# Kernel optimization log

Hardware: AMD Instinct MI355X
Metric: run time of the kernel (lower is better)

The kernel has to match this reference:

```python
import jax, jax.numpy as jnp
import numpy as np

B = 4          # batch (number of point clouds)
NPER = 50000   # voxels per cloud
G = 96         # voxel grid extent per axis
C = 128        # in_channels
R = 2          # reduction_ratio
K = 27         # 3^3 kernel offsets
BN_EPS = 1e-5


def _build_sparse_geometry(seed=0):
    """Unique voxel coords per sample + 27-neighbor kernel map (Minkowski-style)."""
    rng = np.random.default_rng(seed)
    keys_list = []
    for b in range(B):
        loc = rng.choice(G ** 3, NPER, replace=False)
        loc.sort()
        keys_list.append(b * (G ** 3) + loc)
    keys = np.concatenate(keys_list)  # globally sorted (batch-major)
    N = keys.shape[0]
    loc = keys % (G ** 3)
    xs, ys, zs = loc // (G * G), (loc // G) % G, loc % G
    offsets = [(dx, dy, dz) for dx in (-1, 0, 1) for dy in (-1, 0, 1) for dz in (-1, 0, 1)]
    nbr_idx = np.zeros((N, K), np.int32)
    nbr_mask = np.zeros((N, K), bool)
    for k, (dx, dy, dz) in enumerate(offsets):
        inb = ((xs + dx >= 0) & (xs + dx < G) & (ys + dy >= 0) & (ys + dy < G)
               & (zs + dz >= 0) & (zs + dz < G))
        nkey = keys + dx * G * G + dy * G + dz
        pos = np.searchsorted(keys, nkey)
        pos_c = np.clip(pos, 0, N - 1)
        found = inb & (keys[pos_c] == nkey)
        nbr_idx[:, k] = np.where(found, pos_c, 0)
        nbr_mask[:, k] = found
    batch_idx = np.repeat(np.arange(B), NPER).astype(np.int32)
    return nbr_idx, nbr_mask, batch_idx


def setup_inputs() -> dict:
    nbr_idx, nbr_mask, batch_idx = _build_sparse_geometry(0)
    N = B * NPER
    key = jax.random.key(0)
    ks = jax.random.split(key, 8)
    feats = jax.random.normal(ks[0], (N, C), jnp.float32)
    # channel-attention MLP (MinkowskiLinear has bias=True)
    w1 = jax.random.normal(ks[1], (C, C // R), jnp.float32) * (1.0 / np.sqrt(C))
    b1 = jnp.zeros((C // R,), jnp.float32)
    w2 = jax.random.normal(ks[2], (C // R, C), jnp.float32) * (1.0 / np.sqrt(C // R))
    b2 = jnp.zeros((C,), jnp.float32)
    # spatial attention: 3x3x3 sparse conv C->4 (bias=False), BN(4), 1x1x1 conv 4->4
    conv1_w = jax.random.normal(ks[3], (K, C, 4), jnp.float32) * (1.0 / np.sqrt(K * C))
    bn_gamma = jnp.ones((4,), jnp.float32)
    bn_beta = jnp.zeros((4,), jnp.float32)
    conv2_w = jax.random.normal(ks[4], (4, 4), jnp.float32) * 0.5
    return dict(feats=feats, w1=w1, b1=b1, w2=w2, b2=b2, conv1_w=conv1_w,
                bn_gamma=bn_gamma, bn_beta=bn_beta, conv2_w=conv2_w,
                nbr_idx=jnp.asarray(nbr_idx), nbr_mask=jnp.asarray(nbr_mask),
                batch_idx=jnp.asarray(batch_idx), num_batches=B)


def reference(feats, w1, b1, w2, b2, conv1_w, bn_gamma, bn_beta, conv2_w,
              nbr_idx, nbr_mask, batch_idx, num_batches):
    N = feats.shape[0]
    ones = jnp.ones((N,), feats.dtype)
    counts = jax.ops.segment_sum(ones, batch_idx, num_segments=num_batches,
                                 indices_are_sorted=True)  # [B]
    avg_x = jax.ops.segment_sum(feats, batch_idx, num_segments=num_batches,
                                indices_are_sorted=True) / counts[:, None]  # [B,C]
    max_x = jax.ops.segment_max(feats, batch_idx, num_segments=num_batches,
                                indices_are_sorted=True)  # [B,C]
    mlp = lambda z: jax.nn.relu(z @ w1 + b1) @ w2 + b2
    weights = jax.nn.sigmoid(mlp(avg_x) + mlp(max_x))  # [B,C] channel attention
    # sam_mid: per-sample broadcast multiply
    mid = feats * weights[batch_idx]  # [N,C]
    # sparse 3x3x3 conv C->4 via kernel map (gather + thin matmul per offset)
    mask_f = nbr_mask.astype(feats.dtype)
    y = jnp.zeros((N, 4), feats.dtype)
    for k in range(K):
        y = y + (mid[nbr_idx[:, k]] * mask_f[:, k:k + 1]) @ conv1_w[k]
    # BatchNorm (training-mode batch stats, biased var) + ReLU
    mu = jnp.mean(y, axis=0)
    var = jnp.var(y, axis=0)
    y = (y - mu) * jax.lax.rsqrt(var + BN_EPS) * bn_gamma + bn_beta
    y = jax.nn.relu(y)
    # 1x1x1 conv == linear (bias=False), then sigmoid
    final = jax.nn.sigmoid(y @ conv2_w)  # [N,4]
    # sam_output: max over channels -> scalar spatial gate per point
    gate = jnp.max(final, axis=1, keepdims=True)  # [N,1]
    out = mid * gate + mid + feats
    return out
```

## Files before the change

kernel.cpp:

```cpp
#include <hip/hip_runtime.h>

#define C 128
#define K 27
#define BATCHES 4
#define RA_BPB 512
#define CONV_BLOCKS 512
#define CONV_BPB (CONV_BLOCKS / BATCHES)
#define CONV_TPB 1024
#define NWAVES_CONV (CONV_BLOCKS * (CONV_TPB / 64))
#define BN_EPS 1e-5f

typedef __attribute__((ext_vector_type(2))) __fp16 h2;
typedef __attribute__((ext_vector_type(8))) __fp16 h8;

__global__ __launch_bounds__(256) void reduceA_kernel(
    const float* __restrict__ feats, float* __restrict__ psum,
    float* __restrict__ pmax, const unsigned int* __restrict__ mwords,
    int* __restrict__ flag, int NPER) {
  int base = blockIdx.x * 512;
  bool bad = false;
  bad |= (mwords[base + threadIdx.x] > 1u);
  bad |= (mwords[base + 256 + threadIdx.x] > 1u);
  if (__any(bad) && (threadIdx.x & 63) == 0) atomicOr(flag, 1);

  int b = blockIdx.x / RA_BPB, chunk = blockIdx.x % RA_BPB;
  int CH = (NPER + RA_BPB - 1) / RA_BPB;
  int r0 = b * NPER + chunk * CH;
  int r1 = min(b * NPER + NPER, r0 + CH);
  int g = threadIdx.x >> 5;
  int l = threadIdx.x & 31;
  float4 s = make_float4(0.f, 0.f, 0.f, 0.f);
  float4 m = make_float4(-INFINITY, -INFINITY, -INFINITY, -INFINITY);
  int i = r0 + g;
  for (; i + 8 < r1; i += 16) {
    float4 v1 = *(const float4*)(feats + (size_t)i * C + l * 4);
    float4 v2 = *(const float4*)(feats + (size_t)(i + 8) * C + l * 4);
    s.x += v1.x + v2.x; s.y += v1.y + v2.y;
    s.z += v1.z + v2.z; s.w += v1.w + v2.w;
    m.x = fmaxf(m.x, fmaxf(v1.x, v2.x)); m.y = fmaxf(m.y, fmaxf(v1.y, v2.y));
    m.z = fmaxf(m.z, fmaxf(v1.z, v2.z)); m.w = fmaxf(m.w, fmaxf(v1.w, v2.w));
  }
  if (i < r1) {
    float4 v = *(const float4*)(feats + (size_t)i * C + l * 4);
    s.x += v.x; s.y += v.y; s.z += v.z; s.w += v.w;
    m.x = fmaxf(m.x, v.x); m.y = fmaxf(m.y, v.y);
    m.z = fmaxf(m.z, v.z); m.w = fmaxf(m.w, v.w);
  }
  __shared__ float ssum[8][C], smax[8][C];
  *(float4*)&ssum[g][l * 4] = s;
  *(float4*)&smax[g][l * 4] = m;
  __syncthreads();
  if (threadIdx.x < C) {
    int c = threadIdx.x;
    float S = 0.f, M = -INFINITY;
#pragma unroll
    for (int gg = 0; gg < 8; ++gg) {
      S += ssum[gg][c];
      M = fmaxf(M, smax[gg][c]);
    }
    psum[(size_t)blockIdx.x * C + c] = S;
    pmax[(size_t)blockIdx.x * C + c] = M;
  }
}

__global__ __launch_bounds__(256) void reduceB_mlp_kernel(
    const float* __restrict__ psum, const float* __restrict__ pmax,
    const float* __restrict__ w1, const float* __restrict__ b1,
    const float* __restrict__ w2, const float* __restrict__ b2,
    float* __restrict__ wgt, int NPER) {
  int b = blockIdx.x;
  int g = threadIdx.x >> 5, l = threadIdx.x & 31;
  float4 s = make_float4(0.f, 0.f, 0.f, 0.f);
  float4 m = make_float4(-INFINITY, -INFINITY, -INFINITY, -INFINITY);
  for (int j = g; j < RA_BPB; j += 8) {
    size_t base = (size_t)(b * RA_BPB + j) * C + l * 4;
    float4 vs = *(const float4*)(psum + base);
    float4 vm = *(const float4*)(pmax + base);
    s.x += vs.x; s.y += vs.y; s.z += vs.z; s.w += vs.w;
    m.x = fmaxf(m.x, vm.x); m.y = fmaxf(m.y, vm.y);
    m.z = fmaxf(m.z, vm.z); m.w = fmaxf(m.w, vm.w);
  }
  __shared__ float ssum[8][C], smax[8][C];
  *(float4*)&ssum[g][l * 4] = s;
  *(float4*)&smax[g][l * 4] = m;
  __syncthreads();
  __shared__ float avgs[C], mxs[C];
  if (threadIdx.x < C) {
    int c = threadIdx.x;
    float S = 0.f, M = -INFINITY;
#pragma unroll
    for (int gg = 0; gg < 8; ++gg) {
      S += ssum[gg][c];
      M = fmaxf(M, smax[gg][c]);
    }
    avgs[c] = S / (float)NPER;
    mxs[c] = M;
  }
  __syncthreads();
  __shared__ float h1a[64], h1m[64];
  int t = threadIdx.x;
  if (t < 64) {
    float sa = b1[t], sm = b1[t];
    for (int c = 0; c < C; ++c) {
      float wv = w1[c * 64 + t];
      sa += avgs[c] * wv;
      sm += mxs[c] * wv;
    }
    h1a[t] = fmaxf(sa, 0.f);
    h1m[t] = fmaxf(sm, 0.f);
  }
  __syncthreads();
  if (t < C) {
    float za = b2[t], zm = b2[t];
    for (int h = 0; h < 64; ++h) {
      float wv = w2[h * C + t];
      za += h1a[h] * wv;
      zm += h1m[h] * wv;
    }
    float z = za + zm;
    wgt[b * C + t] = 1.f / (1.f + expf(-z));
  }
}

__global__ __launch_bounds__(CONV_TPB, 8) void conv_kernel(
    const float* __restrict__ feats, const float* __restrict__ wgt,
    const float* __restrict__ conv1_w, const int* __restrict__ nbr_idx,
    const void* __restrict__ nbr_mask, const int* __restrict__ flagp,
    float* __restrict__ y, float* __restrict__ bnpart, int N, int NPER) {
  int bat = blockIdx.x / CONV_BPB;
  const float* wgtRow = wgt + bat * C;
  __shared__ __align__(16) h8 wlds[K * 64];
  int tid = threadIdx.x;
  for (int e = tid; e < K * 64; e += CONV_TPB) {
    int l = e & 63;
    float wa = wgtRow[2 * l], wb = wgtRow[2 * l + 1];
    float4 A = ((const float4*)conv1_w)[e * 2];
    float4 B = ((const float4*)conv1_w)[e * 2 + 1];
    h8 w;
    h2 p;
    p = __builtin_amdgcn_cvt_pkrtz(A.x * wa, B.x * wb); w[0] = p[0]; w[1] = p[1];
    p = __builtin_amdgcn_cvt_pkrtz(A.y * wa, B.y * wb); w[2] = p[0]; w[3] = p[1];
    p = __builtin_amdgcn_cvt_pkrtz(A.z * wa, B.z * wb); w[4] = p[0]; w[5] = p[1];
    p = __builtin_amdgcn_cvt_pkrtz(A.w * wa, B.w * wb); w[6] = p[0]; w[7] = p[1];
    wlds[e] = w;
  }
  __syncthreads();

  int lane = tid & 63;
  int g = lane >> 4, cl = lane & 15;
  int gwave = blockIdx.x * (CONV_TPB / 64) + (tid >> 6);
  int wb = (blockIdx.x % CONV_BPB) * (CONV_TPB / 64) + (tid >> 6);
  int wavesPerBatch = CONV_BPB * (CONV_TPB / 64);
  int rpw = (NPER + wavesPerBatch - 1) / wavesPerBatch;
  int rbeg = bat * NPER + wb * rpw;
  int rend = min(bat * NPER + NPER, rbeg + rpw);
  bool byteMode = (*flagp != 0);
  const unsigned char* mb = (const unsigned char*)nbr_mask;
  const int* mi = (const int*)nbr_mask;

  bool mk = false;
  int jl = 0;
  if (rbeg < rend && lane < K) {
    size_t e = (size_t)rbeg * K + lane;
    mk = byteMode ? (mb[e] != 0) : (mi[e] != 0);
    jl = nbr_idx[e];
  }

  float sAcc = 0.f, qAcc = 0.f;

  unsigned balTailN = 0, balTailP = 0;
  int jN = 0, jP = 0, cntN = 0, cntP = 0;
  int k0N = 0, k1N = 0, k2N = 0, k3N = 0, k0P = 0, k1P = 0, k2P = 0, k3P = 0;
  float2 g0N = make_float2(0, 0), g1N = g0N, g2N = g0N, g3N = g0N;
  float2 g0P = g0N, g1P = g0N, g2P = g0N, g3P = g0N;

#define FRONT(iF)                                                           \
  do {                                                                      \
    unsigned bb = (unsigned)__ballot(mk);                                   \
    jN = jl;                                                                \
    mk = false;                                                             \
    if ((iF) + 1 < rend && lane < K) {                                      \
      size_t e = (size_t)((iF) + 1) * K + lane;                             \
      mk = byteMode ? (mb[e] != 0) : (mi[e] != 0);                          \
      jl = nbr_idx[e];                                                      \
    }                                                                       \
    cntN = __popc(bb);                                                      \
    k0N = __ffs(bb) - 1; bb &= bb - 1;                                      \
    k1N = __ffs(bb) - 1; bb &= bb - 1;                                      \
    k2N = __ffs(bb) - 1; bb &= bb - 1;                                      \
    k3N = __ffs(bb) - 1; bb &= bb - 1;                                      \
    balTailN = bb;                                                          \
    int j0 = __shfl(jN, k0N & 63);                                          \
    int j1 = __shfl(jN, k1N & 63);                                          \
    int j2 = __shfl(jN, k2N & 63);                                          \
    int j3 = __shfl(jN, k3N & 63);                                          \
    if (cntN > 0) g0N = *(const float2*)(feats + (size_t)j0 * C + 2 * lane);\
    if (cntN > 1) g1N = *(const float2*)(feats + (size_t)j1 * C + 2 * lane);\
    if (cntN > 2) g2N = *(const float2*)(feats + (size_t)j2 * C + 2 * lane);\
    if (cntN > 3) g3N = *(const float2*)(feats + (size_t)j3 * C + 2 * lane);\
  } while (0)

#define ACCD(ff, kk)                                                        \
  {                                                                         \
    h2 fp = __builtin_amdgcn_cvt_pkrtz(ff.x, ff.y);                         \
    h8 w = wlds[(kk)*64 + lane];                                            \
    h2 w0 = __builtin_shufflevector(w, w, 0, 1);                            \
    h2 w1 = __builtin_shufflevector(w, w, 2, 3);                            \
    h2 w2 = __builtin_shufflevector(w, w, 4, 5);                            \
    h2 w3 = __builtin_shufflevector(w, w, 6, 7);                            \
    a0 = __builtin_amdgcn_fdot2(fp, w0, a0, false);                         \
    a1 = __builtin_amdgcn_fdot2(fp, w1, a1, false);                         \
    a2 = __builtin_amdgcn_fdot2(fp, w2, a2, false);                         \
    a3 = __builtin_amdgcn_fdot2(fp, w3, a3, false);                         \
  }

#define BACK(ir)                                                            \
  do {                                                                      \
    float a0 = 0, a1 = 0, a2 = 0, a3 = 0;                                   \
    if (cntP > 0) ACCD(g0P, k0P)                                            \
    if (cntP > 1) ACCD(g1P, k1P)                                            \
    if (cntP > 2) ACCD(g2P, k2P)                                            \
    if (cntP > 3) ACCD(g3P, k3P)                                            \
    unsigned bt = balTailP;                                                 \
    while (bt) {                                                            \
      int kk = __ffs(bt) - 1; bt &= bt - 1;                                 \
      int jj = __shfl(jP, kk);                                              \
      float2 f = *(const float2*)(feats + (size_t)jj * C + 2 * lane);       \
      ACCD(f, kk)                                                           \
    }                                                                       \
    float u = (g < 2) ? a2 : a0;                                            \
    float vv = (g < 2) ? a3 : a1;                                           \
    float m0 = ((g < 2) ? a0 : a2) + __shfl_xor(u, 32);                     \
    float m1 = ((g < 2) ? a1 : a3) + __shfl_xor(vv, 32);                    \
    float w = (g & 1) ? m0 : m1;                                            \
    float vf = ((g & 1) ? m1 : m0) + __shfl_xor(w, 16);                     \
    vf += __shfl_xor(vf, 1);                                                \
    vf += __shfl_xor(vf, 2);                                                \
    vf += __shfl_xor(vf, 4);                                                \
    vf += __shfl_xor(vf, 8);                                                \
    if (cl == 0) y[(size_t)(ir)*4 + g] = vf;                                \
    sAcc += vf; qAcc += vf * vf;                                            \
  } while (0)

#define ROTATE()                                                            \
  do {                                                                      \
    balTailP = balTailN; jP = jN; cntP = cntN;                              \
    k0P = k0N; k1P = k1N; k2P = k2N; k3P = k3N;                             \
    g0P = g0N; g1P = g1N; g2P = g2N; g3P = g3N;                             \
  } while (0)

  if (rbeg < rend) {
    FRONT(rbeg);
    ROTATE();
    for (int i = rbeg + 1; i < rend; ++i) {
      FRONT(i);
      BACK(i - 1);
      ROTATE();
    }
    BACK(rend - 1);
  }
#undef FRONT
#undef ACCD
#undef BACK
#undef ROTATE

  if (cl == 0) {
    float* p = bnpart + (size_t)gwave * 8;
    p[g] = sAcc;
    p[4 + g] = qAcc;
  }
}

__global__ void bn_reduce_kernel(const float* __restrict__ bnpart, int nparts,
                                 const float* __restrict__ gamma, const float* __restrict__ beta,
                                 float* __restrict__ scsh, int N) {
  __shared__ float red[256 * 8];
  int t = threadIdx.x;
  float S[8];
#pragma unroll
  for (int o = 0; o < 8; ++o) S[o] = 0.f;
  for (int i = t; i < nparts; i += 256) {
#pragma unroll
    for (int o = 0; o < 8; ++o) S[o] += bnpart[(size_t)i * 8 + o];
  }
#pragma unroll
  for (int o = 0; o < 8; ++o) red[t * 8 + o] = S[o];
  __syncthreads();
  for (int st = 128; st > 0; st >>= 1) {
    if (t < st) {
#pragma unroll
      for (int o = 0; o < 8; ++o) red[t * 8 + o] += red[(t + st) * 8 + o];
    }
    __syncthreads();
  }
  if (t == 0) {
    float invN = 1.f / (float)N;
#pragma unroll
    for (int o = 0; o < 4; ++o) {
      float mu = red[o] * invN;
      float var = red[4 + o] * invN - mu * mu;
      float sc = gamma[o] * rsqrtf(var + BN_EPS);
      scsh[o] = sc;
      scsh[4 + o] = beta[o] - mu * sc;
    }
  }
}

__global__ __launch_bounds__(256) void final_kernel(
    const float* __restrict__ feats, const float* __restrict__ wgt,
    const float* __restrict__ y, const float* __restrict__ scsh,
    const float* __restrict__ c2, float* __restrict__ out, int N, int NPER) {
  int lane = threadIdx.x & 63;
  int half = lane >> 5;
  int hl = lane & 31;
  int gwave = blockIdx.x * (blockDim.x >> 6) + (threadIdx.x >> 6);
  int nwaves = gridDim.x * (blockDim.x >> 6);
  int P = (N + 1) >> 1;
  int ppw = (P + nwaves - 1) / nwaves;
  int pbeg = gwave * ppw, pend = min(P, pbeg + ppw);
  if (pbeg >= pend) return;
  float4 sc = *(const float4*)scsh;
  float4 sh = *(const float4*)(scsh + 4);
  float4 r0 = *(const float4*)(c2 + 0);
  float4 r1 = *(const float4*)(c2 + 4);
  float4 r2 = *(const float4*)(c2 + 8);
  float4 r3 = *(const float4*)(c2 + 12);
  int bB = min((2 * pbeg) / NPER, BATCHES - 1);
  int bEnd = (bB + 1) * NPER;
  float4 w = *(const float4*)(wgt + bB * C + hl * 4);

  int i0 = 2 * pbeg + half;
  float4 yvN = make_float4(0, 0, 0, 0), fN = yvN;
  if (i0 < N) {
    yvN = *(const float4*)(y + (size_t)i0 * 4);
    fN = *(const float4*)(feats + (size_t)i0 * C + hl * 4);
  }
  for (int p = pbeg; p < pend; ++p) {
    int i = 2 * p + half;
    float4 yv = yvN;
    float4 f = fN;
    int inext = 2 * (p + 1) + half;
    if (p + 1 < pend && inext < N) {
      yvN = *(const float4*)(y + (size_t)inext * 4);
      fN = *(const float4*)(feats + (size_t)inext * C + hl * 4);
    }
    if (2 * p >= bEnd && bB < BATCHES - 1) {
      ++bB; bEnd += NPER;
      w = *(const float4*)(wgt + bB * C + hl * 4);
    }
    if (i < N) {
      float y0 = fmaxf(yv.x * sc.x + sh.x, 0.f);
      float y1 = fmaxf(yv.y * sc.y + sh.y, 0.f);
      float y2 = fmaxf(yv.z * sc.z + sh.z, 0.f);
      float y3 = fmaxf(yv.w * sc.w + sh.w, 0.f);
      float z0 = y0 * r0.x + y1 * r1.x + y2 * r2.x + y3 * r3.x;
      float z1 = y0 * r0.y + y1 * r1.y + y2 * r2.y + y3 * r3.y;
      float z2 = y0 * r0.z + y1 * r1.z + y2 * r2.z + y3 * r3.z;
      float z3 = y0 * r0.w + y1 * r1.w + y2 * r2.w + y3 * r3.w;
      float zm = fmaxf(fmaxf(z0, z1), fmaxf(z2, z3));
      float gate = 1.f / (1.f + expf(-zm));
      float g1 = 1.f + gate;
      float4 o;
      o.x = f.x * (1.f + w.x * g1);
      o.y = f.y * (1.f + w.y * g1);
      o.z = f.z * (1.f + w.z * g1);
      o.w = f.w * (1.f + w.w * g1);
      *(float4*)(out + (size_t)i * C + hl * 4) = o;
    }
  }
}

extern "C" void kernel_launch(void* const* d_in, const int* in_sizes, int n_in,
                              void* d_out, int out_size, void* d_ws, size_t ws_size,
                              hipStream_t stream) {
  const float* feats   = (const float*)d_in[0];
  const float* w1      = (const float*)d_in[1];
  const float* b1      = (const float*)d_in[2];
  const float* w2      = (const float*)d_in[3];
  const float* b2      = (const float*)d_in[4];
  const float* conv1w  = (const float*)d_in[5];
  const float* gamma   = (const float*)d_in[6];
  const float* beta    = (const float*)d_in[7];
  const float* c2      = (const float*)d_in[8];
  const int*   nbr_idx = (const int*)d_in[9];
  const void*  nbr_mask = d_in[10];
  int N = in_sizes[0] / C;
  int NPER = N / BATCHES;

  char* ws = (char*)d_ws;
  size_t off = 0;
  int* flag = (int*)(ws + off);        off += 16;
  float* psum = (float*)(ws + off);    off += (size_t)BATCHES * RA_BPB * C * 4;
  float* pmax = (float*)(ws + off);    off += (size_t)BATCHES * RA_BPB * C * 4;
  float* wgt  = (float*)(ws + off);    off += (size_t)BATCHES * C * 4;
  float* y    = (float*)(ws + off);    off += (size_t)N * 4 * 4;
  float* bnpart = (float*)(ws + off);  off += (size_t)NWAVES_CONV * 8 * 4;
  float* scsh = (float*)(ws + off);    off += 64;
  float* outp = (float*)d_out;

  hipMemsetAsync(flag, 0, sizeof(int), stream);
  reduceA_kernel<<<BATCHES * RA_BPB, 256, 0, stream>>>(
      feats, psum, pmax, (const unsigned int*)nbr_mask, flag, NPER);
  reduceB_mlp_kernel<<<BATCHES, 256, 0, stream>>>(psum, pmax, w1, b1, w2, b2, wgt, NPER);
  conv_kernel<<<CONV_BLOCKS, CONV_TPB, 0, stream>>>(feats, wgt, conv1w, nbr_idx, nbr_mask,
                                                    flag, y, bnpart, N, NPER);
  bn_reduce_kernel<<<1, 256, 0, stream>>>(bnpart, NWAVES_CONV, gamma, beta, scsh, N);
  final_kernel<<<2048, 256, 0, stream>>>(feats, wgt, y, scsh, c2, outp, N, NPER);
}
```

Before: 151.1 us.

## Fold MLP and BN-reduce kernels into predecessors via last-block ticket

The channel-attention MLP reduction is folded into reduceA_kernel, and the BatchNorm statistics reduction is folded into conv_kernel. In each case an atomic ticket elects the last finishing block to do the final work. Conv blocks now pre-reduce per-wave stats in shared memory and atomically add them into a global 8-float accumulator. This removes two kernel launches and their launch gaps. In exchange, the MLP for all four batches runs serially in a single block, and float atomics make the BN sums order-nondeterministic.

After: 522.8 us. 246% more time.

```diff
diff --git a/kernel.cpp b/kernel.cpp
--- a/kernel.cpp
+++ b/kernel.cpp
@@ -7,7 +7,6 @@
 #define CONV_BLOCKS 512
 #define CONV_BPB (CONV_BLOCKS / BATCHES)
 #define CONV_TPB 1024
-#define NWAVES_CONV (CONV_BLOCKS * (CONV_TPB / 64))
 #define BN_EPS 1e-5f
 
 typedef __attribute__((ext_vector_type(2))) __fp16 h2;
@@ -16,7 +15,10 @@
 __global__ __launch_bounds__(256) void reduceA_kernel(
     const float* __restrict__ feats, float* __restrict__ psum,
     float* __restrict__ pmax, const unsigned int* __restrict__ mwords,
-    int* __restrict__ flag, int NPER) {
+    int* __restrict__ flag, int* __restrict__ ticket,
+    const float* __restrict__ w1, const float* __restrict__ b1,
+    const float* __restrict__ w2, const float* __restrict__ b2,
+    float* __restrict__ wgt, int NPER) {
   int base = blockIdx.x * 512;
   bool bad = false;
   bad |= (mwords[base + threadIdx.x] > 1u);
@@ -61,64 +63,66 @@
     psum[(size_t)blockIdx.x * C + c] = S;
     pmax[(size_t)blockIdx.x * C + c] = M;
   }
-}
-
-__global__ __launch_bounds__(256) void reduceB_mlp_kernel(
-    const float* __restrict__ psum, const float* __restrict__ pmax,
-    const float* __restrict__ w1, const float* __restrict__ b1,
-    const float* __restrict__ w2, const float* __restrict__ b2,
-    float* __restrict__ wgt, int NPER) {
-  int b = blockIdx.x;
-  int g = threadIdx.x >> 5, l = threadIdx.x & 31;
-  float4 s = make_float4(0.f, 0.f, 0.f, 0.f);
-  float4 m = make_float4(-INFINITY, -INFINITY, -INFINITY, -INFINITY);
-  for (int j = g; j < RA_BPB; j += 8) {
-    size_t base = (size_t)(b * RA_BPB + j) * C + l * 4;
-    float4 vs = *(const float4*)(psum + base);
-    float4 vm = *(const float4*)(pmax + base);
-    s.x += vs.x; s.y += vs.y; s.z += vs.z; s.w += vs.w;
-    m.x = fmaxf(m.x, vm.x); m.y = fmaxf(m.y, vm.y);
-    m.z = fmaxf(m.z, vm.z); m.w = fmaxf(m.w, vm.w);
-  }
-  __shared__ float ssum[8][C], smax[8][C];
-  *(float4*)&ssum[g][l * 4] = s;
-  *(float4*)&smax[g][l * 4] = m;
+
+  __threadfence();
+  __shared__ int isLast;
+  if (threadIdx.x == 0)
+    isLast = (atomicAdd(ticket, 1) == (int)gridDim.x - 1);
   __syncthreads();
-  __shared__ float avgs[C], mxs[C];
-  if (threadIdx.x < C) {
-    int c = threadIdx.x;
-    float S = 0.f, M = -INFINITY;
+  if (!isLast) return;
+  __threadfence();
+
+  __shared__ float avgs[C], mxs[C], h1a[64], h1m[64];
+  int t = threadIdx.x;
+  for (int bb = 0; bb < BATCHES; ++bb) {
+    int gg = t >> 5, ll = t & 31;
+    float4 s4 = make_float4(0.f, 0.f, 0.f, 0.f);
+    float4 m4 = make_float4(-INFINITY, -INFINITY, -INFINITY, -INFINITY);
+    for (int j = gg; j < RA_BPB; j += 8) {
+      size_t bs = (size_t)(bb * RA_BPB + j) * C + ll * 4;
+      float4 vs = *(const float4*)(psum + bs);
+      float4 vm = *(const float4*)(pmax + bs);
+      s4.x += vs.x; s4.y += vs.y; s4.z += vs.z; s4.w += vs.w;
+      m4.x = fmaxf(m4.x, vm.x); m4.y = fmaxf(m4.y, vm.y);
+      m4.z = fmaxf(m4.z, vm.z); m4.w = fmaxf(m4.w, vm.w);
+    }
+    __syncthreads();
+    *(float4*)&ssum[gg][ll * 4] = s4;
+    *(float4*)&smax[gg][ll * 4] = m4;
+    __syncthreads();
+    if (t < C) {
+      float S = 0.f, M = -INFINITY;
 #pragma unroll
-    for (int gg = 0; gg < 8; ++gg) {
-      S += ssum[gg][c];
-      M = fmaxf(M, smax[gg][c]);
-    }
-    avgs[c] = S / (float)NPER;
-    mxs[c] = M;
-  }
-  __syncthreads();
-  __shared__ float h1a[64], h1m[64];
-  int t = threadIdx.x;
-  if (t < 64) {
-    float sa = b1[t], sm = b1[t];
-    for (int c = 0; c < C; ++c) {
-      float wv = w1[c * 64 + t];
-      sa += avgs[c] * wv;
-      sm += mxs[c] * wv;
-    }
-    h1a[t] = fmaxf(sa, 0.f);
-    h1m[t] = fmaxf(sm, 0.f);
-  }
-  __syncthreads();
-  if (t < C) {
-    float za = b2[t], zm = b2[t];
-    for (int h = 0; h < 64; ++h) {
-      float wv = w2[h * C + t];
-      za += h1a[h] * wv;
-      zm += h1m[h] * wv;
-    }
-    float z = za + zm;
-    wgt[b * C + t] = 1.f / (1.f + expf(-z));
+      for (int g8 = 0; g8 < 8; ++g8) {
+        S += ssum[g8][t];
+        M = fmaxf(M, smax[g8][t]);
+      }
+      avgs[t] = S / (float)NPER;
+      mxs[t] = M;
+    }
+    __syncthreads();
+    if (t < 64) {
+      float sa = b1[t], sm = b1[t];
+      for (int c = 0; c < C; ++c) {
+        float wv = w1[c * 64 + t];
+        sa += avgs[c] * wv;
+        sm += mxs[c] * wv;
+      }
+      h1a[t] = fmaxf(sa, 0.f);
+      h1m[t] = fmaxf(sm, 0.f);
+    }
+    __syncthreads();
+    if (t < C) {
+      float za = b2[t], zm = b2[t];
+      for (int h = 0; h < 64; ++h) {
+        float wv = w2[h * C + t];
+        za += h1a[h] * wv;
+        zm += h1m[h] * wv;
+      }
+      float z = za + zm;
+      wgt[bb * C + t] = 1.f / (1.f + expf(-z));
+    }
+    __syncthreads();
   }
 }
 
@@ -126,30 +130,33 @@
     const float* __restrict__ feats, const float* __restrict__ wgt,
     const float* __restrict__ conv1_w, const int* __restrict__ nbr_idx,
     const void* __restrict__ nbr_mask, const int* __restrict__ flagp,
-    float* __restrict__ y, float* __restrict__ bnpart, int N, int NPER) {
+    float* __restrict__ y, float* __restrict__ stats, int* __restrict__ ticket,
+    const float* __restrict__ gamma, const float* __restrict__ beta,
+    float* __restrict__ scsh, int N, int NPER) {
   int bat = blockIdx.x / CONV_BPB;
   const float* wgtRow = wgt + bat * C;
   __shared__ __align__(16) h8 wlds[K * 64];
+  __shared__ float wstat[16][8];
   int tid = threadIdx.x;
   for (int e = tid; e < K * 64; e += CONV_TPB) {
     int l = e & 63;
-    float wa = wgtRow[2 * l], wb = wgtRow[2 * l + 1];
+    float wa = wgtRow[2 * l], wb_ = wgtRow[2 * l + 1];
     float4 A = ((const float4*)conv1_w)[e * 2];
     float4 B = ((const float4*)conv1_w)[e * 2 + 1];
     h8 w;
     h2 p;
-    p = __builtin_amdgcn_cvt_pkrtz(A.x * wa, B.x * wb); w[0] = p[0]; w[1] = p[1];
-    p = __builtin_amdgcn_cvt_pkrtz(A.y * wa, B.y * wb); w[2] = p[0]; w[3] = p[1];
-    p = __builtin_amdgcn_cvt_pkrtz(A.z * wa, B.z * wb); w[4] = p[0]; w[5] = p[1];
-    p = __builtin_amdgcn_cvt_pkrtz(A.w * wa, B.w * wb); w[6] = p[0]; w[7] = p[1];
+    p = __builtin_amdgcn_cvt_pkrtz(A.x * wa, B.x * wb_); w[0] = p[0]; w[1] = p[1];
+    p = __builtin_amdgcn_cvt_pkrtz(A.y * wa, B.y * wb_); w[2] = p[0]; w[3] = p[1];
+    p = __builtin_amdgcn_cvt_pkrtz(A.z * wa, B.z * wb_); w[4] = p[0]; w[5] = p[1];
+    p = __builtin_amdgcn_cvt_pkrtz(A.w * wa, B.w * wb_); w[6] = p[0]; w[7] = p[1];
     wlds[e] = w;
   }
   __syncthreads();
 
   int lane = tid & 63;
   int g = lane >> 4, cl = lane & 15;
-  int gwave = blockIdx.x * (CONV_TPB / 64) + (tid >> 6);
-  int wb = (blockIdx.x % CONV_BPB) * (CONV_TPB / 64) + (tid >> 6);
+  int waveId = tid >> 6;
+  int wb = (blockIdx.x % CONV_BPB) * (CONV_TPB / 64) + waveId;
   int wavesPerBatch = CONV_BPB * (CONV_TPB / 64);
   int rpw = (NPER + wavesPerBatch - 1) / wavesPerBatch;
   int rbeg = bat * NPER + wb * rpw;
@@ -265,44 +272,30 @@
 #undef ROTATE
 
   if (cl == 0) {
-    float* p = bnpart + (size_t)gwave * 8;
-    p[g] = sAcc;
-    p[4 + g] = qAcc;
-  }
-}
-
-__global__ void bn_reduce_kernel(const float* __restrict__ bnpart, int nparts,
-                                 const float* __restrict__ gamma, const float* __restrict__ beta,
-                                 float* __restrict__ scsh, int N) {
-  __shared__ float red[256 * 8];
-  int t = threadIdx.x;
-  float S[8];
+    wstat[waveId][g] = sAcc;
+    wstat[waveId][4 + g] = qAcc;
+  }
+  __syncthreads();
+  if (tid < 8) {
+    float t = 0.f;
 #pragma unroll
-  for (int o = 0; o < 8; ++o) S[o] = 0.f;
-  for (int i = t; i < nparts; i += 256) {
-#pragma unroll
-    for (int o = 0; o < 8; ++o) S[o] += bnpart[(size_t)i * 8 + o];
-  }
-#pragma unroll
-  for (int o = 0; o < 8; ++o) red[t * 8 + o] = S[o];
+    for (int w = 0; w < 16; ++w) t += wstat[w][tid];
+    atomicAdd(&stats[tid], t);
+  }
+  __threadfence();
+  __shared__ int isLast;
+  if (tid == 0)
+    isLast = (atomicAdd(ticket, 1) == (int)gridDim.x - 1);
   __syncthreads();
-  for (int st = 128; st > 0; st >>= 1) {
-    if (t < st) {
-#pragma unroll
-      for (int o = 0; o < 8; ++o) red[t * 8 + o] += red[(t + st) * 8 + o];
-    }
-    __syncthreads();
-  }
-  if (t == 0) {
+  if (isLast && tid < 4) {
     float invN = 1.f / (float)N;
-#pragma unroll
-    for (int o = 0; o < 4; ++o) {
-      float mu = red[o] * invN;
-      float var = red[4 + o] * invN - mu * mu;
-      float sc = gamma[o] * rsqrtf(var + BN_EPS);
-      scsh[o] = sc;
-      scsh[4 + o] = beta[o] - mu * sc;
-    }
+    float su = atomicAdd(&stats[tid], 0.f);
+    float sq = atomicAdd(&stats[4 + tid], 0.f);
+    float mu = su * invN;
+    float var = sq * invN - mu * mu;
+    float sc = gamma[tid] * rsqrtf(var + BN_EPS);
+    scsh[tid] = sc;
+    scsh[4 + tid] = beta[tid] - mu * sc;
   }
 }
 
@@ -388,22 +381,24 @@
   int NPER = N / BATCHES;
 
   char* ws = (char*)d_ws;
-  size_t off = 0;
-  int* flag = (int*)(ws + off);        off += 16;
+  int* flag     = (int*)(ws + 0);
+  int* ticketA  = (int*)(ws + 4);
+  int* ticketC  = (int*)(ws + 8);
+  float* stats  = (float*)(ws + 16);
+  size_t off = 64;
   float* psum = (float*)(ws + off);    off += (size_t)BATCHES * RA_BPB * C * 4;
   float* pmax = (float*)(ws + off);    off += (size_t)BATCHES * RA_BPB * C * 4;
   float* wgt  = (float*)(ws + off);    off += (size_t)BATCHES * C * 4;
   float* y    = (float*)(ws + off);    off += (size_t)N * 4 * 4;
-  float* bnpart = (float*)(ws + off);  off += (size_t)NWAVES_CONV * 8 * 4;
   float* scsh = (float*)(ws + off);    off += 64;
   float* outp = (float*)d_out;
 
-  hipMemsetAsync(flag, 0, sizeof(int), stream);
+  hipMemsetAsync(ws, 0, 64, stream);
   reduceA_kernel<<<BATCHES * RA_BPB, 256, 0, stream>>>(
-      feats, psum, pmax, (const unsigned int*)nbr_mask, flag, NPER);
-  reduceB_mlp_kernel<<<BATCHES, 256, 0, stream>>>(psum, pmax, w1, b1, w2, b2, wgt, NPER);
-  conv_kernel<<<CONV_BLOCKS, CONV_TPB, 0, stream>>>(feats, wgt, conv1w, nbr_idx, nbr_mask,
-                                                    flag, y, bnpart, N, NPER);
-  bn_reduce_kernel<<<1, 256, 0, stream>>>(bnpart, NWAVES_CONV, gamma, beta, scsh, N);
+      feats, psum, pmax, (const unsigned int*)nbr_mask, flag, ticketA,
+      w1, b1, w2, b2, wgt, NPER);
+  conv_kernel<<<CONV_BLOCKS, CONV_TPB, 0, stream>>>(
+      feats, wgt, conv1w, nbr_idx, nbr_mask, flag, y, stats, ticketC,
+      gamma, beta, scsh, N, NPER);
   final_kernel<<<2048, 256, 0, stream>>>(feats, wgt, y, scsh, c2, outp, N, NPER);
 }
```
